# Kernel optimization log

Measured on AMD Instinct MI355X. Metric: run time of the kernel, lower is better.

Reference implementation:

```python
import jax, jax.numpy as jnp
import numpy as np

N = 50000
E = 800000


def _lin(x, w, b):
    return x @ w.T + b


def _gat(h, src, dst, w, a_src, a_dst, b):
    # Single-head PyG-style GATConv (heads=1, negative_slope=0.2), self-loops added by caller.
    n = h.shape[0]
    hw = h @ w.T                                              # [n, out]
    logit = jax.nn.leaky_relu((hw @ a_src)[src] + (hw @ a_dst)[dst], negative_slope=0.2)  # [e]
    m = jax.ops.segment_max(logit, dst, num_segments=n)
    m = jax.lax.stop_gradient(jnp.where(jnp.isfinite(m), m, 0.0))
    ex = jnp.exp(logit - m[dst])
    denom = jax.ops.segment_sum(ex, dst, num_segments=n)
    alpha = ex / (denom[dst] + 1e-16)                          # segment softmax over incoming edges
    return jax.ops.segment_sum(alpha[:, None] * hw[src], dst, num_segments=n) + b


def _forward(x_all, edge_index,
             sep1_w, sep1_b, sep2_w, sep2_b, sep3_w, sep3_b, sep4_w, sep4_b,
             sep5_w, sep5_b, sep6_w, sep6_b, sep7_w, sep7_b, sep8_w, sep8_b,
             conv1_w, conv1_as, conv1_ad, conv1_b,
             conv2_w, conv2_as, conv2_ad, conv2_b,
             conv3_w, conv3_as, conv3_ad, conv3_b,
             lstm_wih, lstm_whh, lstm_bih, lstm_bhh,
             lin1_w, lin1_b, lin2_w, lin2_b, lin3_w, lin3_b):
    n = x_all.shape[0]
    loops = jnp.arange(n)
    src = jnp.concatenate([edge_index[0], loops])  # GATConv default add_self_loops=True
    dst = jnp.concatenate([edge_index[1], loops])
    relu, sig = jax.nn.relu, jax.nn.sigmoid
    xr = relu(_lin(sig(_lin(x_all[:, 1:3],    sep1_w, sep1_b)), sep5_w, sep5_b))   # [n,64]
    xl = relu(_lin(sig(_lin(x_all[:, 3:16],   sep2_w, sep2_b)), sep6_w, sep6_b))   # [n,64]
    xs = relu(_lin(sig(_lin(x_all[:, 16:56],  sep3_w, sep3_b)), sep7_w, sep7_b))   # [n,128]
    xv = relu(_lin(sig(_lin(x_all[:, 56:421], sep4_w, sep4_b)), sep8_w, sep8_b))   # [n,128]
    x = jnp.concatenate([xr, xl, xs, xv], axis=1)                                  # [n,384]
    x = relu(_gat(x, src, dst, conv1_w, conv1_as, conv1_ad, conv1_b))              # [n,128]
    x = relu(_gat(x, src, dst, conv2_w, conv2_as, conv2_ad, conv2_b))              # [n,128]
    x = relu(_gat(x, src, dst, conv3_w, conv3_as, conv3_ad, conv3_b))              # [n,64]
    # LSTM with seq_len=1, h0=c0=0 -> a single cell step; W_hh term vanishes (h0=0)
    t = x_all[:, 421:441]                                                          # [n,20]
    gates = t @ lstm_wih.T + lstm_bih + lstm_bhh                                   # [n,256]
    i, f, g, o = jnp.split(gates, 4, axis=1)                                       # torch gate order i,f,g,o
    c = sig(i) * jnp.tanh(g)
    h = sig(o) * jnp.tanh(c)                                                       # [n,64]
    x = jnp.concatenate([x, h], axis=1)                                            # [n,128]
    x = relu(_lin(x, lin1_w, lin1_b))
    x = relu(_lin(x, lin2_w, lin2_b))
    return _lin(x, lin3_w, lin3_b)                                                 # [n,56]


def setup_inputs() -> dict:
    key = jax.random.key(0)
    ks = iter(jax.random.split(key, 64))
    def w(shape, scale=0.05):
        return jax.random.normal(next(ks), shape, dtype=jnp.float32) * scale
    inp = {
        'x_all': jax.random.normal(next(ks), (N, 441), dtype=jnp.float32),
        'edge_index': jax.random.randint(next(ks), (2, E), 0, N),
        'sep1_w': w((64, 2)),    'sep1_b': w((64,)),
        'sep2_w': w((64, 13)),   'sep2_b': w((64,)),
        'sep3_w': w((128, 40)),  'sep3_b': w((128,)),
        'sep4_w': w((128, 365)), 'sep4_b': w((128,)),
        'sep5_w': w((64, 64)),   'sep5_b': w((64,)),
        'sep6_w': w((64, 64)),   'sep6_b': w((64,)),
        'sep7_w': w((128, 128)), 'sep7_b': w((128,)),
        'sep8_w': w((128, 128)), 'sep8_b': w((128,)),
        'conv1_w': w((128, 384)), 'conv1_as': w((128,)), 'conv1_ad': w((128,)), 'conv1_b': w((128,)),
        'conv2_w': w((128, 128)), 'conv2_as': w((128,)), 'conv2_ad': w((128,)), 'conv2_b': w((128,)),
        'conv3_w': w((64, 128)),  'conv3_as': w((64,)),  'conv3_ad': w((64,)),  'conv3_b': w((64,)),
        'lstm_wih': w((256, 20)), 'lstm_whh': w((256, 64)), 'lstm_bih': w((256,)), 'lstm_bhh': w((256,)),
        'lin1_w': w((64, 128)), 'lin1_b': w((64,)),
        'lin2_w': w((64, 64)),  'lin2_b': w((64,)),
        'lin3_w': w((56, 64)),  'lin3_b': w((56,)),
    }
    return inp


def reference(x_all, edge_index,
              sep1_w, sep1_b, sep2_w, sep2_b, sep3_w, sep3_b, sep4_w, sep4_b,
              sep5_w, sep5_b, sep6_w, sep6_b, sep7_w, sep7_b, sep8_w, sep8_b,
              conv1_w, conv1_as, conv1_ad, conv1_b,
              conv2_w, conv2_as, conv2_ad, conv2_b,
              conv3_w, conv3_as, conv3_ad, conv3_b,
              lstm_wih, lstm_whh, lstm_bih, lstm_bhh,
              lin1_w, lin1_b, lin2_w, lin2_b, lin3_w, lin3_b):
    return _forward(x_all, edge_index,
                    sep1_w, sep1_b, sep2_w, sep2_b, sep3_w, sep3_b, sep4_w, sep4_b,
                    sep5_w, sep5_b, sep6_w, sep6_b, sep7_w, sep7_b, sep8_w, sep8_b,
                    conv1_w, conv1_as, conv1_ad, conv1_b,
                    conv2_w, conv2_as, conv2_ad, conv2_b,
                    conv3_w, conv3_as, conv3_ad, conv3_b,
                    lstm_wih, lstm_whh, lstm_bih, lstm_bhh,
                    lin1_w, lin1_b, lin2_w, lin2_b, lin3_w, lin3_b)
```

## Files before the change

kernel.cpp:

```cpp
#include <hip/hip_runtime.h>
#include <hip/hip_bf16.h>
#include <math.h>

#define N_NODES 50000
#define N_EDGES 800000
#define NP 50048
#define RB16 (NP / 16)

typedef __hip_bfloat16 bf16;
typedef __attribute__((ext_vector_type(8))) short short8;
typedef __attribute__((ext_vector_type(4))) float f32x4;

__device__ __forceinline__ float lrelu(float x) { return x > 0.f ? x : 0.2f * x; }

__device__ __forceinline__ short f2b(float v) {
    bf16 h = __float2bfloat16(v);
    return *reinterpret_cast<short*>(&h);
}
__device__ __forceinline__ float lo_bf(unsigned u) { return __uint_as_float(u << 16); }
__device__ __forceinline__ float hi_bf(unsigned u) { return __uint_as_float(u & 0xFFFF0000u); }
__device__ __forceinline__ float b2f_s(unsigned short s) {
    return __uint_as_float(((unsigned)s) << 16);
}
__device__ __forceinline__ unsigned pack_bf(float v0, float v1) {
    unsigned a = (unsigned)(unsigned short)f2b(v0);
    unsigned b = (unsigned)(unsigned short)f2b(v1);
    return a | (b << 16);
}
__device__ __forceinline__ float sigm(float x) { return 1.f / (1.f + expf(-x)); }

__device__ __forceinline__ size_t fm_idx(int row, int c, int KIo) {
    return ((size_t)(row >> 4) * KIo + (c >> 5)) * 512 +
           (size_t)((c >> 3) & 3) * 128 + (size_t)(row & 15) * 8 + (c & 7);
}

template <int KI, int K, int OFF>
__device__ __forceinline__ void pack_x_body(const float* __restrict__ x,
                                            short* __restrict__ out, int nrows,
                                            long long t)
{
    int lane = (int)(t & 63);
    long long rem = t >> 6;
    int ki = (int)(rem % KI);
    int rb = (int)(rem / KI);
    if (rb >= RB16) return;
    int r = rb * 16 + (lane & 15);
    int kb = ki * 32 + (lane >> 4) * 8;
    short8 tmp;
    if (r < nrows && kb + 8 <= K) {
        const float* p = x + (size_t)r * 441 + OFF + kb;
        f32x4 a = *(const f32x4*)p;
        f32x4 b = *(const f32x4*)(p + 4);
#pragma unroll
        for (int j = 0; j < 4; j++) tmp[j] = f2b(a[j]);
#pragma unroll
        for (int j = 0; j < 4; j++) tmp[4 + j] = f2b(b[j]);
    } else if (r < nrows && kb < K) {
        const float* p = x + (size_t)r * 441 + OFF + kb;
#pragma unroll
        for (int j = 0; j < 8; j++) tmp[j] = (kb + j < K) ? f2b(p[j]) : (short)0;
    } else {
#pragma unroll
        for (int j = 0; j < 8; j++) tmp[j] = 0;
    }
    *(short8*)(out + (((size_t)rb * KI + ki) * 64 + lane) * 8) = tmp;
}

__global__ __launch_bounds__(256) void pack_x2_kernel(
    const float* __restrict__ x, short* __restrict__ xs4,
    short* __restrict__ xs3, int nrows)
{
    long long t = (long long)blockIdx.x * 256 + threadIdx.x;
    const long long T4 = (long long)RB16 * 12 * 64;
    if (t < T4) pack_x_body<12, 365, 56>(x, xs4, nrows, t);
    else        pack_x_body<2, 40, 16>(x, xs3, nrows, t - T4);
}

struct PackDesc {
    const float* src;
    short* dst;
    int lda, M, K, CT, KI;
};
struct PackArgs {
    PackDesc d[16];
    unsigned long long sz[16];
    int n;
};

__global__ __launch_bounds__(256) void pack_all_kernel(PackArgs pa,
                                                       unsigned long long total)
{
    for (unsigned long long i =
             (unsigned long long)blockIdx.x * blockDim.x + threadIdx.x;
         i < total; i += (unsigned long long)gridDim.x * blockDim.x) {
        unsigned long long off = i;
        int s = 0;
        while (s < pa.n - 1 && off >= pa.sz[s]) { off -= pa.sz[s]; s++; }
        PackDesc D = pa.d[s];
        int j = (int)(off & 7);
        int lane = (int)((off >> 3) & 63);
        unsigned rem = (unsigned)(off >> 9);
        int ct = rem % (unsigned)D.CT;
        int ki = rem / (unsigned)D.CT;
        int r = ct * 16 + (lane & 15);
        int k = ki * 32 + (lane >> 4) * 8 + j;
        float v = (r < D.M && k < D.K) ? D.src[(size_t)r * D.lda + k] : 0.f;
        D.dst[off] = f2b(v);
    }
}

template <int ACT, int ODT, int CT, int KI, int SCORES>
__global__ __launch_bounds__(256) void dgemm_kernel(
    const short* __restrict__ A,
    const short* __restrict__ W,
    const float* __restrict__ bias,
    void* __restrict__ Cv, int ldc, int nrows, int M,
    const float* __restrict__ a_src, const float* __restrict__ a_dst,
    float* __restrict__ ssrc, float* __restrict__ sdst)
{
    int tid = threadIdx.x;
    int row0 = blockIdx.x * 64;
    int wv = tid >> 6, lane = tid & 63;
    int lrow = lane & 15, quad = lane >> 4;

    const short* Ap = A + ((size_t)((row0 >> 4) + wv) * KI) * 512 + (size_t)lane * 8;
    const short* Wp = W + (size_t)lane * 8;

    short8 areg[KI];
#pragma unroll
    for (int ki = 0; ki < KI; ki++) areg[ki] = *(const short8*)(Ap + (size_t)ki * 512);

    f32x4 acc[CT];
#pragma unroll
    for (int ct = 0; ct < CT; ct++)
#pragma unroll
        for (int i = 0; i < 4; i++) acc[ct][i] = 0.f;

#pragma unroll
    for (int ki = 0; ki < KI; ki++) {
        short8 breg[CT];
#pragma unroll
        for (int ct = 0; ct < CT; ct++)
            breg[ct] = *(const short8*)(Wp + ((size_t)ki * CT + ct) * 512);
#pragma unroll
        for (int ct = 0; ct < CT; ct++)
            acc[ct] = __builtin_amdgcn_mfma_f32_16x16x32_bf16(areg[ki], breg[ct], acc[ct], 0, 0, 0);
    }

    float* Cf = (float*)Cv;
    bf16*  Cb = (bf16*)Cv;
#pragma unroll
    for (int ct = 0; ct < CT; ct++) {
        int gcol = ct * 16 + lrow;
        if (gcol >= M) continue;
        float bv = bias ? bias[gcol] : 0.f;
#pragma unroll
        for (int i = 0; i < 4; i++) {
            int grow = row0 + wv * 16 + quad * 4 + i;
            if (grow >= nrows) continue;
            float v = acc[ct][i] + bv;
            if (ACT == 1) v = fmaxf(v, 0.f);
            if (ACT == 2) v = sigm(v);
            if (ODT == 1) Cb[(size_t)grow * ldc + gcol] = __float2bfloat16(v);
            else          Cf[(size_t)grow * ldc + gcol] = v;
        }
    }

    if (SCORES) {
        float as_c[CT], ad_c[CT];
#pragma unroll
        for (int ct = 0; ct < CT; ct++) {
            int gcol = ct * 16 + lrow;
            as_c[ct] = (gcol < M) ? a_src[gcol] : 0.f;
            ad_c[ct] = (gcol < M) ? a_dst[gcol] : 0.f;
        }
#pragma unroll
        for (int i = 0; i < 4; i++) {
            float ps = 0.f, pd = 0.f;
#pragma unroll
            for (int ct = 0; ct < CT; ct++) {
                ps = fmaf(acc[ct][i], as_c[ct], ps);
                pd = fmaf(acc[ct][i], ad_c[ct], pd);
            }
#pragma unroll
            for (int off = 8; off > 0; off >>= 1) {
                ps += __shfl_down(ps, off);
                pd += __shfl_down(pd, off);
            }
            if (lrow == 0) {
                int grow = row0 + wv * 16 + quad * 4 + i;
                if (grow < nrows) { ssrc[grow] = ps; sdst[grow] = pd; }
            }
        }
    }
}

template <int ADT, int CT1, int CT2, int KI1>
__device__ __forceinline__ void brmlp_body(
    short* sH,
    const void* __restrict__ Av, int lda, int aoff,
    const short* __restrict__ W1p, const float* __restrict__ B1,
    const short* __restrict__ W2p, const float* __restrict__ B2,
    short* __restrict__ out, int KIo, int coff, int nrows, int K1)
{
    constexpr int M1 = CT1 * 16;
    constexpr int LDH = M1 + 8;
    constexpr int KI2 = M1 / 32;

    int tid = threadIdx.x;
    int row0 = blockIdx.x * 64;
    int wv = tid >> 6, lane = tid & 63;
    int lrow = lane & 15, quad = lane >> 4;

    {
        short8 areg[KI1];
        if (ADT == 1) {
            const short* As = (const short*)Av +
                              ((size_t)((row0 >> 4) + wv) * KI1) * 512 + (size_t)lane * 8;
#pragma unroll
            for (int ki = 0; ki < KI1; ki++)
                areg[ki] = *(const short8*)(As + (size_t)ki * 512);
        } else {
            const float* Af = (const float*)Av;
            int arow = row0 + wv * 16 + lrow;
            bool rok = arow < nrows;
#pragma unroll
            for (int ki = 0; ki < KI1; ki++)
#pragma unroll
                for (int j = 0; j < 8; j++) {
                    int k = ki * 32 + quad * 8 + j;
                    areg[ki][j] = (rok && k < K1)
                                      ? f2b(Af[(size_t)arow * lda + aoff + k])
                                      : (short)0;
                }
        }

        f32x4 acc[CT1];
#pragma unroll
        for (int ct = 0; ct < CT1; ct++)
#pragma unroll
            for (int i = 0; i < 4; i++) acc[ct][i] = 0.f;

#pragma unroll
        for (int ki = 0; ki < KI1; ki++) {
            short8 breg[CT1];
#pragma unroll
            for (int ct = 0; ct < CT1; ct++)
                breg[ct] = *(const short8*)(W1p + ((size_t)ki * CT1 + ct) * 512 +
                                            (size_t)lane * 8);
#pragma unroll
            for (int ct = 0; ct < CT1; ct++)
                acc[ct] = __builtin_amdgcn_mfma_f32_16x16x32_bf16(areg[ki], breg[ct], acc[ct], 0, 0, 0);
        }
#pragma unroll
        for (int ct = 0; ct < CT1; ct++) {
            int col = ct * 16 + lrow;
            float bv = B1[col];
#pragma unroll
            for (int i = 0; i < 4; i++)
                sH[(wv * 16 + quad * 4 + i) * LDH + col] = f2b(sigm(acc[ct][i] + bv));
        }
    }

    {
        f32x4 acc[CT2];
#pragma unroll
        for (int ct = 0; ct < CT2; ct++)
#pragma unroll
            for (int i = 0; i < 4; i++) acc[ct][i] = 0.f;

#pragma unroll
        for (int ki = 0; ki < KI2; ki++) {
            short8 a = *(short8*)&sH[(wv * 16 + lrow) * LDH + ki * 32 + quad * 8];
            short8 breg[CT2];
#pragma unroll
            for (int ct = 0; ct < CT2; ct++)
                breg[ct] = *(const short8*)(W2p + ((size_t)ki * CT2 + ct) * 512 +
                                            (size_t)lane * 8);
#pragma unroll
            for (int ct = 0; ct < CT2; ct++)
                acc[ct] = __builtin_amdgcn_mfma_f32_16x16x32_bf16(a, breg[ct], acc[ct], 0, 0, 0);
        }
#pragma unroll
        for (int ct = 0; ct < CT2; ct++) {
            int gcol = ct * 16 + lrow;
            float bv = B2[gcol];
            int c = coff + gcol;
#pragma unroll
            for (int i = 0; i < 4; i++) {
                int grow = row0 + wv * 16 + quad * 4 + i;
                if (grow >= nrows) continue;
                float v = fmaxf(acc[ct][i] + bv, 0.f);
                out[fm_idx(grow, c, KIo)] = f2b(v);
            }
        }
    }
}

template <int ADT, int CT1, int CT2, int KI1>
__global__ __launch_bounds__(256) void brmlp_kernel(
    const void* __restrict__ Av, int lda, int aoff,
    const short* __restrict__ W1p, const float* __restrict__ B1,
    const short* __restrict__ W2p, const float* __restrict__ B2,
    short* __restrict__ out, int KIo, int coff, int nrows, int K1)
{
    __shared__ short sH[64 * (CT1 * 16 + 8)];
    brmlp_body<ADT, CT1, CT2, KI1>(sH, Av, lda, aoff, W1p, B1, W2p, B2,
                                   out, KIo, coff, nrows, K1);
}

__global__ __launch_bounds__(256) void brmlp_pair_kernel(
    const void* __restrict__ Av, int lda,
    const short* __restrict__ W1a, const float* __restrict__ B1a,
    const short* __restrict__ W2a, const float* __restrict__ B2a,
    const short* __restrict__ W1b, const float* __restrict__ B1b,
    const short* __restrict__ W2b, const float* __restrict__ B2b,
    short* __restrict__ out, int KIo, int nrows)
{
    __shared__ short sH[64 * 72];
    if (blockIdx.y == 0)
        brmlp_body<0, 4, 4, 1>(sH, Av, lda, 1, W1a, B1a, W2a, B2a,
                               out, KIo, 0, nrows, 2);
    else
        brmlp_body<0, 4, 4, 1>(sH, Av, lda, 3, W1b, B1b, W2b, B2b,
                               out, KIo, 64, nrows, 13);
}

__global__ __launch_bounds__(256) void head_kernel(
    const short* __restrict__ xgs, const float* __restrict__ x_all,
    const float* __restrict__ wih, const float* __restrict__ bih,
    const float* __restrict__ bhh,
    const short* __restrict__ w1p, const float* __restrict__ b1,
    const short* __restrict__ w2p, const float* __restrict__ b2,
    const short* __restrict__ w3p, const float* __restrict__ b3,
    float* __restrict__ dout, int n)
{
    __shared__ short sW[20][200];
    __shared__ float sT[64][20];
    __shared__ short sH[64][72];
    __shared__ short sH2[64][72];
    __shared__ short sH3[64][72];

    int tid = threadIdx.x;
    int row0 = blockIdx.x * 64;
    int wv = tid >> 6, lane = tid & 63;
    int lrow = lane & 15, quad = lane >> 4;

    short8 axg[2];
#pragma unroll
    for (int ki = 0; ki < 2; ki++)
        axg[ki] = *(const short8*)(xgs + (((size_t)((row0 >> 4) + wv) * 2 + ki) * 64 +
                                          lane) * 8);

    for (int i = tid; i < 20 * 192; i += 256) {
        int k = i / 192, j = i % 192;
        int gate = j >> 6, jj = j & 63;
        int srow = (gate == 0) ? jj : (gate == 1 ? 128 + jj : 192 + jj);
        sW[k][j] = f2b(wih[srow * 20 + k]);
    }
    for (int i = tid; i < 64 * 20; i += 256) {
        int r = i / 20, k = i % 20;
        int grow = row0 + r;
        sT[r][k] = (grow < n) ? x_all[(size_t)grow * 441 + 421 + k] : 0.f;
    }
    __syncthreads();

    for (int p = 0; p < 16; p++) {
        int idx = p * 256 + tid;
        int r = idx >> 6, j = idx & 63;
        float gi = 0.f, gg = 0.f, go = 0.f;
#pragma unroll
        for (int k = 0; k < 20; k++) {
            float t = sT[r][k];
            gi = fmaf(t, b2f_s((unsigned short)sW[k][j]), gi);
            gg = fmaf(t, b2f_s((unsigned short)sW[k][64 + j]), gg);
            go = fmaf(t, b2f_s((unsigned short)sW[k][128 + j]), go);
        }
        gi += bih[j] + bhh[j];
        gg += bih[128 + j] + bhh[128 + j];
        go += bih[192 + j] + bhh[192 + j];
        float c = sigm(gi) * tanhf(gg);
        float h = sigm(go) * tanhf(c);
        sH[r][j] = f2b(h);
    }
    __syncthreads();

    f32x4 acc[4];
#pragma unroll
    for (int ct = 0; ct < 4; ct++)
#pragma unroll
        for (int i = 0; i < 4; i++) acc[ct][i] = 0.f;
#pragma unroll
    for (int ki = 0; ki < 4; ki++) {
        short8 a = (ki < 2) ? axg[ki]
                            : *(short8*)&sH[wv * 16 + lrow][(ki - 2) * 32 + quad * 8];
        short8 breg[4];
#pragma unroll
        for (int ct = 0; ct < 4; ct++)
            breg[ct] = *(const short8*)(w1p + ((size_t)ki * 4 + ct) * 512 +
                                        (size_t)lane * 8);
#pragma unroll
        for (int ct = 0; ct < 4; ct++)
            acc[ct] = __builtin_amdgcn_mfma_f32_16x16x32_bf16(a, breg[ct], acc[ct], 0, 0, 0);
    }
#pragma unroll
    for (int ct = 0; ct < 4; ct++) {
        int col = ct * 16 + lrow;
        float bv = b1[col];
#pragma unroll
        for (int i = 0; i < 4; i++)
            sH2[wv * 16 + quad * 4 + i][col] = f2b(fmaxf(acc[ct][i] + bv, 0.f));
    }

#pragma unroll
    for (int ct = 0; ct < 4; ct++)
#pragma unroll
        for (int i = 0; i < 4; i++) acc[ct][i] = 0.f;
#pragma unroll
    for (int ki = 0; ki < 2; ki++) {
        short8 a = *(short8*)&sH2[wv * 16 + lrow][ki * 32 + quad * 8];
        short8 breg[4];
#pragma unroll
        for (int ct = 0; ct < 4; ct++)
            breg[ct] = *(const short8*)(w2p + ((size_t)ki * 4 + ct) * 512 +
                                        (size_t)lane * 8);
#pragma unroll
        for (int ct = 0; ct < 4; ct++)
            acc[ct] = __builtin_amdgcn_mfma_f32_16x16x32_bf16(a, breg[ct], acc[ct], 0, 0, 0);
    }
#pragma unroll
    for (int ct = 0; ct < 4; ct++) {
        int col = ct * 16 + lrow;
        float bv = b2[col];
#pragma unroll
        for (int i = 0; i < 4; i++)
            sH3[wv * 16 + quad * 4 + i][col] = f2b(fmaxf(acc[ct][i] + bv, 0.f));
    }

#pragma unroll
    for (int ct = 0; ct < 4; ct++)
#pragma unroll
        for (int i = 0; i < 4; i++) acc[ct][i] = 0.f;
#pragma unroll
    for (int ki = 0; ki < 2; ki++) {
        short8 a = *(short8*)&sH3[wv * 16 + lrow][ki * 32 + quad * 8];
        short8 breg[4];
#pragma unroll
        for (int ct = 0; ct < 4; ct++)
            breg[ct] = *(const short8*)(w3p + ((size_t)ki * 4 + ct) * 512 +
                                        (size_t)lane * 8);
#pragma unroll
        for (int ct = 0; ct < 4; ct++)
            acc[ct] = __builtin_amdgcn_mfma_f32_16x16x32_bf16(a, breg[ct], acc[ct], 0, 0, 0);
    }
#pragma unroll
    for (int ct = 0; ct < 4; ct++) {
        int gcol = ct * 16 + lrow;
        if (gcol >= 56) continue;
        float bv = b3[gcol];
#pragma unroll
        for (int i = 0; i < 4; i++) {
            int grow = row0 + wv * 16 + quad * 4 + i;
            if (grow >= n) continue;
            dout[(size_t)grow * 56 + gcol] = acc[ct][i] + bv;
        }
    }
}

template <int FPL, int KIo>
__global__ __launch_bounds__(256) void gat_fused_kernel(
    const bf16* __restrict__ hw, const int* __restrict__ rowptr,
    const int* __restrict__ colidx, const float* __restrict__ ss,
    const float* __restrict__ sd, const float* __restrict__ bias,
    short* __restrict__ out, int n, int F)
{
    int wv = threadIdx.x >> 6, lane = threadIdx.x & 63;
    int node = blockIdx.x * 4 + wv;
    if (node >= n) return;
    const unsigned short* hwu = (const unsigned short*)hw;
    float sdn = sd[node];
    float wself = expf(lrelu(ss[node] + sdn));
    float a0, a1 = 0.f;
    if (FPL == 2) {
        unsigned u = *(const unsigned*)(hwu + (size_t)node * F + 2 * lane);
        a0 = wself * lo_bf(u);
        a1 = wself * hi_bf(u);
    } else {
        a0 = wself * b2f_s(hwu[(size_t)node * F + lane]);
    }
    int e0 = rowptr[node];
    int deg = rowptr[node + 1] - e0;
    float den_l = 0.f;
    for (int c0 = 0; c0 < deg; c0 += 64) {
        int mye = c0 + lane;
        int s = 0;
        float w = 0.f;
        if (mye < deg) {
            s = colidx[e0 + mye];
            w = expf(lrelu(ss[s] + sdn));
        }
        den_l += w;
        int cnt = min(64, deg - c0);
        int j = 0;
        for (; j + 7 < cnt; j += 8) {
            int sx[8];
            float wx[8];
#pragma unroll
            for (int q = 0; q < 8; q++) {
                sx[q] = __shfl(s, j + q);
                wx[q] = __shfl(w, j + q);
            }
            if (FPL == 2) {
                unsigned ux[8];
#pragma unroll
                for (int q = 0; q < 8; q++)
                    ux[q] = *(const unsigned*)(hwu + (size_t)sx[q] * F + 2 * lane);
#pragma unroll
                for (int q = 0; q < 8; q++) {
                    a0 = fmaf(wx[q], lo_bf(ux[q]), a0);
                    a1 = fmaf(wx[q], hi_bf(ux[q]), a1);
                }
            } else {
                float hx[8];
#pragma unroll
                for (int q = 0; q < 8; q++)
                    hx[q] = b2f_s(hwu[(size_t)sx[q] * F + lane]);
#pragma unroll
                for (int q = 0; q < 8; q++) a0 = fmaf(wx[q], hx[q], a0);
            }
        }
        for (; j + 3 < cnt; j += 4) {
            int s0 = __shfl(s, j), s1 = __shfl(s, j + 1);
            int s2 = __shfl(s, j + 2), s3 = __shfl(s, j + 3);
            float w0 = __shfl(w, j), w1v = __shfl(w, j + 1);
            float w2v = __shfl(w, j + 2), w3v = __shfl(w, j + 3);
            if (FPL == 2) {
                unsigned u0 = *(const unsigned*)(hwu + (size_t)s0 * F + 2 * lane);
                unsigned u1 = *(const unsigned*)(hwu + (size_t)s1 * F + 2 * lane);
                unsigned u2 = *(const unsigned*)(hwu + (size_t)s2 * F + 2 * lane);
                unsigned u3 = *(const unsigned*)(hwu + (size_t)s3 * F + 2 * lane);
                a0 = fmaf(w0, lo_bf(u0), a0);  a1 = fmaf(w0, hi_bf(u0), a1);
                a0 = fmaf(w1v, lo_bf(u1), a0); a1 = fmaf(w1v, hi_bf(u1), a1);
                a0 = fmaf(w2v, lo_bf(u2), a0); a1 = fmaf(w2v, hi_bf(u2), a1);
                a0 = fmaf(w3v, lo_bf(u3), a0); a1 = fmaf(w3v, hi_bf(u3), a1);
            } else {
                float h0 = b2f_s(hwu[(size_t)s0 * F + lane]);
                float h1 = b2f_s(hwu[(size_t)s1 * F + lane]);
                float h2 = b2f_s(hwu[(size_t)s2 * F + lane]);
                float h3 = b2f_s(hwu[(size_t)s3 * F + lane]);
                a0 = fmaf(w0, h0, a0);
                a0 = fmaf(w1v, h1, a0);
                a0 = fmaf(w2v, h2, a0);
                a0 = fmaf(w3v, h3, a0);
            }
        }
        for (; j < cnt; j++) {
            int s0 = __shfl(s, j);
            float w0 = __shfl(w, j);
            if (FPL == 2) {
                unsigned u0 = *(const unsigned*)(hwu + (size_t)s0 * F + 2 * lane);
                a0 = fmaf(w0, lo_bf(u0), a0);
                a1 = fmaf(w0, hi_bf(u0), a1);
            } else {
                a0 = fmaf(w0, b2f_s(hwu[(size_t)s0 * F + lane]), a0);
            }
        }
    }
#pragma unroll
    for (int off = 32; off > 0; off >>= 1) den_l += __shfl_xor(den_l, off);
    float inv = 1.f / (den_l + wself);
    int rb = node >> 4, nr = node & 15;
    if (FPL == 2) {
        float v0 = fmaxf(a0 * inv + bias[2 * lane], 0.f);
        float v1 = fmaxf(a1 * inv + bias[2 * lane + 1], 0.f);
        size_t uidx = ((size_t)rb * KIo + (lane >> 4)) * 256 +
                      (size_t)((lane >> 2) & 3) * 64 + nr * 4 + (lane & 3);
        ((unsigned*)out)[uidx] = pack_bf(v0, v1);
    } else {
        float v0 = fmaxf(a0 * inv + bias[lane], 0.f);
        size_t sidx = ((size_t)rb * KIo + (lane >> 5)) * 512 +
                      (size_t)((lane >> 3) & 3) * 128 + nr * 8 + (lane & 7);
        out[sidx] = f2b(v0);
    }
}

__global__ void count_kernel(const int* __restrict__ dst, int* __restrict__ cnt,
                             int e)
{
    for (int i = blockIdx.x * blockDim.x + threadIdx.x; i < e;
         i += gridDim.x * blockDim.x)
        atomicAdd(cnt + dst[i], 1);
}

#define SCAN_BLOCKS 256

__global__ __launch_bounds__(256) void scan_local_kernel(
    const int* __restrict__ cnt, int* __restrict__ rowptr,
    int* __restrict__ bsum, int n, int chunk)
{
    __shared__ int tmp[256];
    int b = blockIdx.x, tid = threadIdx.x;
    int i = b * chunk + tid;
    int v = (tid < chunk && i < n) ? cnt[i] : 0;
    tmp[tid] = v;
    __syncthreads();
    for (int off = 1; off < 256; off <<= 1) {
        int t = (tid >= off) ? tmp[tid - off] : 0;
        __syncthreads();
        tmp[tid] += t;
        __syncthreads();
    }
    if (tid < chunk && i < n) rowptr[i] = tmp[tid] - v;
    if (tid == 255) bsum[b] = tmp[255];
}

__global__ __launch_bounds__(256) void scan_bsums_kernel(
    int* __restrict__ bsum, int* __restrict__ rowptr, int n)
{
    __shared__ int tmp[256];
    int tid = threadIdx.x;
    int v = bsum[tid];
    tmp[tid] = v;
    __syncthreads();
    for (int off = 1; off < 256; off <<= 1) {
        int t = (tid >= off) ? tmp[tid - off] : 0;
        __syncthreads();
        tmp[tid] += t;
        __syncthreads();
    }
    bsum[tid] = tmp[tid] - v;
    if (tid == 255) rowptr[n] = tmp[255];
}

__global__ __launch_bounds__(256) void scan_add_kernel(
    int* __restrict__ rowptr, int* __restrict__ nextp,
    const int* __restrict__ bsum, int n, int chunk)
{
    int b = blockIdx.x, tid = threadIdx.x;
    int i = b * chunk + tid;
    if (tid < chunk && i < n) {
        int v = rowptr[i] + bsum[b];
        rowptr[i] = v;
        nextp[i] = v;
    }
}

__global__ void fill_kernel(const int* __restrict__ src,
                            const int* __restrict__ dst,
                            int* __restrict__ nextp, int* __restrict__ colidx,
                            int e)
{
    for (int i = blockIdx.x * blockDim.x + threadIdx.x; i < e;
         i += gridDim.x * blockDim.x) {
        int pos = atomicAdd(nextp + dst[i], 1);
        colidx[pos] = src[i];
    }
}

extern "C" void kernel_launch(void* const* d_in, const int* in_sizes, int n_in,
                              void* d_out, int out_size, void* d_ws,
                              size_t ws_size, hipStream_t stream)
{
    const int N = N_NODES;
    const int E = N_EDGES;

    const float* x_all = (const float*)d_in[0];
    const int* edges = (const int*)d_in[1];
    const int* e_src = edges;
    const int* e_dst = edges + E;

    const float* sep1_w = (const float*)d_in[2];  const float* sep1_b = (const float*)d_in[3];
    const float* sep2_w = (const float*)d_in[4];  const float* sep2_b = (const float*)d_in[5];
    const float* sep3_w = (const float*)d_in[6];  const float* sep3_b = (const float*)d_in[7];
    const float* sep4_w = (const float*)d_in[8];  const float* sep4_b = (const float*)d_in[9];
    const float* sep5_w = (const float*)d_in[10]; const float* sep5_b = (const float*)d_in[11];
    const float* sep6_w = (const float*)d_in[12]; const float* sep6_b = (const float*)d_in[13];
    const float* sep7_w = (const float*)d_in[14]; const float* sep7_b = (const float*)d_in[15];
    const float* sep8_w = (const float*)d_in[16]; const float* sep8_b = (const float*)d_in[17];
    const float* conv1_w = (const float*)d_in[18];
    const float* conv1_as = (const float*)d_in[19];
    const float* conv1_ad = (const float*)d_in[20];
    const float* conv1_b = (const float*)d_in[21];
    const float* conv2_w = (const float*)d_in[22];
    const float* conv2_as = (const float*)d_in[23];
    const float* conv2_ad = (const float*)d_in[24];
    const float* conv2_b = (const float*)d_in[25];
    const float* conv3_w = (const float*)d_in[26];
    const float* conv3_as = (const float*)d_in[27];
    const float* conv3_ad = (const float*)d_in[28];
    const float* conv3_b = (const float*)d_in[29];
    const float* lstm_wih = (const float*)d_in[30];
    const float* lstm_bih = (const float*)d_in[32];
    const float* lstm_bhh = (const float*)d_in[33];
    const float* lin1_w = (const float*)d_in[34]; const float* lin1_b = (const float*)d_in[35];
    const float* lin2_w = (const float*)d_in[36]; const float* lin2_b = (const float*)d_in[37];
    const float* lin3_w = (const float*)d_in[38]; const float* lin3_b = (const float*)d_in[39];

    char* ws = (char*)d_ws;
    size_t off = 0;
    auto alloc = [&](size_t bytes) {
        void* p = ws + off;
        off += (bytes + 255) & ~(size_t)255;
        return p;
    };
    short* x0 = (short*)alloc((size_t)NP * 384 * 2);
    short* Bb = (short*)alloc((size_t)NP * 128 * 2);
    float* ssrc = (float*)alloc((size_t)N * 4);
    float* sdst = (float*)alloc((size_t)N * 4);
    int* rowptr = (int*)alloc((size_t)(N + 1) * 4);
    int* nextp  = (int*)alloc((size_t)N * 4);
    int* cnt    = (int*)alloc((size_t)N * 4);
    int* bsum   = (int*)alloc((size_t)SCAN_BLOCKS * 4);
    int* colidx = (int*)alloc((size_t)E * 4);

    short* conv1p = (short*)alloc((size_t)128 * 384 * 2);
    short* conv2p = (short*)alloc((size_t)128 * 128 * 2);
    short* conv3p = (short*)alloc((size_t)64 * 128 * 2);
    short* sep1p  = (short*)alloc((size_t)64 * 32 * 2);
    short* sep2p  = (short*)alloc((size_t)64 * 32 * 2);
    short* sep3p  = (short*)alloc((size_t)128 * 64 * 2);
    short* sep4p  = (short*)alloc((size_t)128 * 384 * 2);
    short* sep5p  = (short*)alloc((size_t)64 * 64 * 2);
    short* sep6p  = (short*)alloc((size_t)64 * 64 * 2);
    short* sep7p  = (short*)alloc((size_t)128 * 128 * 2);
    short* sep8p  = (short*)alloc((size_t)128 * 128 * 2);
    short* lin1p  = (short*)alloc((size_t)64 * 128 * 2);
    short* lin2p  = (short*)alloc((size_t)64 * 64 * 2);
    short* lin3p  = (short*)alloc((size_t)64 * 64 * 2);

    size_t need_xs = off + (size_t)NP * 64 * 2 + (size_t)NP * 384 * 2 + 1024;
    bool packx = ws_size >= need_xs;
    short* xs3 = packx ? (short*)alloc((size_t)NP * 64 * 2) : nullptr;
    short* xs4 = packx ? (short*)alloc((size_t)NP * 384 * 2) : nullptr;

    short* C  = x0;
    short* xg = x0;

    dim3 blk(256);
    int gx = NP / 64;
    int nb4 = (N + 3) / 4;
    int chunk = (N + SCAN_BLOCKS - 1) / SCAN_BLOCKS;

    hipMemsetAsync(cnt, 0, (size_t)N * 4, stream);
    count_kernel<<<1024, 256, 0, stream>>>(e_dst, cnt, E);
    scan_local_kernel<<<SCAN_BLOCKS, 256, 0, stream>>>(cnt, rowptr, bsum, N, chunk);
    scan_bsums_kernel<<<1, 256, 0, stream>>>(bsum, rowptr, N);
    scan_add_kernel<<<SCAN_BLOCKS, 256, 0, stream>>>(rowptr, nextp, bsum, N, chunk);
    fill_kernel<<<1024, 256, 0, stream>>>(e_src, e_dst, nextp, colidx, E);

    if (packx) {
        long long tot = (long long)RB16 * 14 * 64;
        pack_x2_kernel<<<(int)((tot + 255) / 256), blk, 0, stream>>>(
            x_all, xs4, xs3, N);
    }
    {
        PackArgs pa{};
        unsigned long long total = 0;
        int np = 0;
        auto addp = [&](const float* src, short* dst, int lda, int M, int K,
                        int CT, int KI) {
            pa.d[np].src = src; pa.d[np].dst = dst; pa.d[np].lda = lda;
            pa.d[np].M = M; pa.d[np].K = K; pa.d[np].CT = CT; pa.d[np].KI = KI;
            pa.sz[np] = (unsigned long long)CT * KI * 512;
            total += pa.sz[np];
            np++;
        };
        addp(conv1_w, conv1p, 384, 128, 384, 8, 12);
        addp(sep4_w, sep4p, 365, 128, 365, 8, 12);
        addp(conv2_w, conv2p, 128, 128, 128, 8, 4);
        addp(sep7_w, sep7p, 128, 128, 128, 8, 4);
        addp(sep8_w, sep8p, 128, 128, 128, 8, 4);
        addp(conv3_w, conv3p, 128, 64, 128, 4, 4);
        addp(lin1_w, lin1p, 128, 64, 128, 4, 4);
        addp(sep3_w, sep3p, 40, 128, 40, 8, 2);
        addp(sep5_w, sep5p, 64, 64, 64, 4, 2);
        addp(sep6_w, sep6p, 64, 64, 64, 4, 2);
        addp(lin2_w, lin2p, 64, 64, 64, 4, 2);
        addp(lin3_w, lin3p, 64, 56, 64, 4, 2);
        addp(sep1_w, sep1p, 2, 64, 2, 4, 1);
        addp(sep2_w, sep2p, 13, 64, 13, 4, 1);
        pa.n = np;
        pack_all_kernel<<<512, 256, 0, stream>>>(pa, total);
    }

    brmlp_pair_kernel<<<dim3(gx, 2), blk, 0, stream>>>(
        x_all, 441, sep1p, sep1_b, sep5p, sep5_b,
        sep2p, sep2_b, sep6p, sep6_b, x0, 12, N);
    if (packx) {
        brmlp_kernel<1, 8, 8, 2><<<gx, blk, 0, stream>>>(
            xs3, 64, 0, sep3p, sep3_b, sep7p, sep7_b, x0, 12, 128, N, 64);
        brmlp_kernel<1, 8, 8, 12><<<gx, blk, 0, stream>>>(
            xs4, 384, 0, sep4p, sep4_b, sep8p, sep8_b, x0, 12, 256, N, 384);
    } else {
        brmlp_kernel<0, 8, 8, 2><<<gx, blk, 0, stream>>>(
            x_all, 441, 16, sep3p, sep3_b, sep7p, sep7_b, x0, 12, 128, N, 40);
        brmlp_kernel<0, 8, 8, 12><<<gx, blk, 0, stream>>>(
            x_all, 441, 56, sep4p, sep4_b, sep8p, sep8_b, x0, 12, 256, N, 365);
    }

    dgemm_kernel<0, 1, 8, 12, 1><<<gx, blk, 0, stream>>>(
        x0, conv1p, nullptr, Bb, 128, N, 128,
        conv1_as, conv1_ad, ssrc, sdst);
    gat_fused_kernel<2, 4><<<nb4, 256, 0, stream>>>(
        (const bf16*)Bb, rowptr, colidx, ssrc, sdst, conv1_b, C, N, 128);

    dgemm_kernel<0, 1, 8, 4, 1><<<gx, blk, 0, stream>>>(
        C, conv2p, nullptr, Bb, 128, N, 128,
        conv2_as, conv2_ad, ssrc, sdst);
    gat_fused_kernel<2, 4><<<nb4, 256, 0, stream>>>(
        (const bf16*)Bb, rowptr, colidx, ssrc, sdst, conv2_b, C, N, 128);

    dgemm_kernel<0, 1, 4, 4, 1><<<gx, blk, 0, stream>>>(
        C, conv3p, nullptr, Bb, 64, N, 64,
        conv3_as, conv3_ad, ssrc, sdst);
    gat_fused_kernel<1, 2><<<nb4, 256, 0, stream>>>(
        (const bf16*)Bb, rowptr, colidx, ssrc, sdst, conv3_b, xg, N, 64);

    head_kernel<<<gx, blk, 0, stream>>>(
        xg, x_all, lstm_wih, lstm_bih, lstm_bhh,
        lin1p, lin1_b, lin2p, lin2_b, lin3p, lin3_b,
        (float*)d_out, N);
}
```

Measured before the change: 564.6 us.

## Build CSR via two-level bucket partition instead of global atomic counting sort

Replaces the global-atomic count, three-pass scan and scatter-fill CSR build with a bucketed approach. A shared-memory histogram over 256-node buckets and a single-block scan are followed by a partition of (src,dst) pairs into buckets. A per-bucket kernel then does a local count, scan and scatter into colidx. This targets the cost of global atomics and scattered writes. It needs an extra 8-byte-per-edge pairs buffer and only runs when workspace allows, otherwise it falls back to the old path.

```diff
diff --git a/kernel.cpp b/kernel.cpp
--- a/kernel.cpp
+++ b/kernel.cpp
@@ -6,6 +6,7 @@
 #define N_EDGES 800000
 #define NP 50048
 #define RB16 (NP / 16)
+#define NB 196
 
 typedef __hip_bfloat16 bf16;
 typedef __attribute__((ext_vector_type(8))) short short8;
@@ -581,6 +582,111 @@
         size_t sidx = ((size_t)rb * KIo + (lane >> 5)) * 512 +
                       (size_t)((lane >> 3) & 3) * 128 + nr * 8 + (lane & 7);
         out[sidx] = f2b(v0);
+    }
+}
+
+__global__ __launch_bounds__(256) void bhist_kernel(const int* __restrict__ dst,
+                                                    int* __restrict__ bcnt, int e)
+{
+    __shared__ int l[NB];
+    for (int i = threadIdx.x; i < NB; i += 256) l[i] = 0;
+    __syncthreads();
+    for (int i = blockIdx.x * blockDim.x + threadIdx.x; i < e;
+         i += gridDim.x * blockDim.x)
+        atomicAdd(&l[dst[i] >> 8], 1);
+    __syncthreads();
+    for (int i = threadIdx.x; i < NB; i += 256)
+        if (l[i]) atomicAdd(&bcnt[i], l[i]);
+}
+
+__global__ __launch_bounds__(256) void bscan_kernel(
+    const int* __restrict__ bcnt, int* __restrict__ boff,
+    int* __restrict__ bcur, int* __restrict__ rowptr, int n, int e)
+{
+    __shared__ int tmp[256];
+    int tid = threadIdx.x;
+    int v = (tid < NB) ? bcnt[tid] : 0;
+    tmp[tid] = v;
+    __syncthreads();
+    for (int off = 1; off < 256; off <<= 1) {
+        int t = (tid >= off) ? tmp[tid - off] : 0;
+        __syncthreads();
+        tmp[tid] += t;
+        __syncthreads();
+    }
+    int excl = tmp[tid] - v;
+    if (tid < NB) { boff[tid] = excl; bcur[tid] = excl; }
+    if (tid == 0) { boff[NB] = e; rowptr[n] = e; }
+}
+
+__global__ __launch_bounds__(256) void bpart_kernel(
+    const int* __restrict__ src, const int* __restrict__ dst,
+    int* __restrict__ bcur, int2* __restrict__ pairs, int e)
+{
+    __shared__ int lcnt[NB];
+    __shared__ int lbase[NB];
+    const int TILE = 2048;
+    for (long long t0 = (long long)blockIdx.x * TILE; t0 < e;
+         t0 += (long long)gridDim.x * TILE) {
+        for (int i = threadIdx.x; i < NB; i += 256) lcnt[i] = 0;
+        __syncthreads();
+        int rank[8], bb[8], sv[8], dv[8];
+#pragma unroll
+        for (int k = 0; k < 8; k++) {
+            int i = (int)t0 + k * 256 + threadIdx.x;
+            bb[k] = -1;
+            if (i < e) {
+                int d = dst[i];
+                sv[k] = src[i];
+                dv[k] = d;
+                bb[k] = d >> 8;
+                rank[k] = atomicAdd(&lcnt[bb[k]], 1);
+            }
+        }
+        __syncthreads();
+        for (int i = threadIdx.x; i < NB; i += 256)
+            lbase[i] = lcnt[i] ? atomicAdd(&bcur[i], lcnt[i]) : 0;
+        __syncthreads();
+#pragma unroll
+        for (int k = 0; k < 8; k++)
+            if (bb[k] >= 0)
+                pairs[(size_t)lbase[bb[k]] + rank[k]] = make_int2(sv[k], dv[k]);
+        __syncthreads();
+    }
+}
+
+__global__ __launch_bounds__(256) void bcsr_kernel(
+    const int2* __restrict__ pairs, const int* __restrict__ boff,
+    int* __restrict__ rowptr, int* __restrict__ colidx, int n)
+{
+    __shared__ int ncnt[256];
+    __shared__ int tmp[256];
+    int tid = threadIdx.x, b = blockIdx.x;
+    int base = boff[b], end = boff[b + 1];
+    ncnt[tid] = 0;
+    __syncthreads();
+    for (int i = base + tid; i < end; i += 256)
+        atomicAdd(&ncnt[pairs[i].y & 255], 1);
+    __syncthreads();
+    int v = ncnt[tid];
+    tmp[tid] = v;
+    __syncthreads();
+    for (int off = 1; off < 256; off <<= 1) {
+        int t = (tid >= off) ? tmp[tid - off] : 0;
+        __syncthreads();
+        tmp[tid] += t;
+        __syncthreads();
+    }
+    int excl = base + tmp[tid] - v;
+    int node = (b << 8) + tid;
+    if (node < n) rowptr[node] = excl;
+    __syncthreads();
+    ncnt[tid] = excl;
+    __syncthreads();
+    for (int i = base + tid; i < end; i += 256) {
+        int2 p = pairs[i];
+        int pos = atomicAdd(&ncnt[p.y & 255], 1);
+        colidx[pos] = p.x;
     }
 }
 
@@ -712,6 +818,9 @@
     int* cnt    = (int*)alloc((size_t)N * 4);
     int* bsum   = (int*)alloc((size_t)SCAN_BLOCKS * 4);
     int* colidx = (int*)alloc((size_t)E * 4);
+    int* bcnt   = (int*)alloc((size_t)NB * 4);
+    int* boff   = (int*)alloc((size_t)(NB + 1) * 4);
+    int* bcur   = (int*)alloc((size_t)NB * 4);
 
     short* conv1p = (short*)alloc((size_t)128 * 384 * 2);
     short* conv2p = (short*)alloc((size_t)128 * 128 * 2);
@@ -733,20 +842,33 @@
     short* xs3 = packx ? (short*)alloc((size_t)NP * 64 * 2) : nullptr;
     short* xs4 = packx ? (short*)alloc((size_t)NP * 384 * 2) : nullptr;
 
+    size_t need_pairs = off + (size_t)E * 8 + 1024;
+    bool binfill = ws_size >= need_pairs;
+    int2* pairs = binfill ? (int2*)alloc((size_t)E * 8) : nullptr;
+
     short* C  = x0;
     short* xg = x0;
 
     dim3 blk(256);
     int gx = NP / 64;
     int nb4 = (N + 3) / 4;
-    int chunk = (N + SCAN_BLOCKS - 1) / SCAN_BLOCKS;
-
-    hipMemsetAsync(cnt, 0, (size_t)N * 4, stream);
-    count_kernel<<<1024, 256, 0, stream>>>(e_dst, cnt, E);
-    scan_local_kernel<<<SCAN_BLOCKS, 256, 0, stream>>>(cnt, rowptr, bsum, N, chunk);
-    scan_bsums_kernel<<<1, 256, 0, stream>>>(bsum, rowptr, N);
-    scan_add_kernel<<<SCAN_BLOCKS, 256, 0, stream>>>(rowptr, nextp, bsum, N, chunk);
-    fill_kernel<<<1024, 256, 0, stream>>>(e_src, e_dst, nextp, colidx, E);
+
+    if (binfill) {
+        hipMemsetAsync(bcnt, 0, (size_t)NB * 4, stream);
+        bhist_kernel<<<1024, 256, 0, stream>>>(e_dst, bcnt, E);
+        bscan_kernel<<<1, 256, 0, stream>>>(bcnt, boff, bcur, rowptr, N, E);
+        bpart_kernel<<<(E + 2047) / 2048, 256, 0, stream>>>(e_src, e_dst, bcur,
+                                                            pairs, E);
+        bcsr_kernel<<<NB, 256, 0, stream>>>(pairs, boff, rowptr, colidx, N);
+    } else {
+        int chunk = (N + SCAN_BLOCKS - 1) / SCAN_BLOCKS;
+        hipMemsetAsync(cnt, 0, (size_t)N * 4, stream);
+        count_kernel<<<1024, 256, 0, stream>>>(e_dst, cnt, E);
+        scan_local_kernel<<<SCAN_BLOCKS, 256, 0, stream>>>(cnt, rowptr, bsum, N, chunk);
+        scan_bsums_kernel<<<1, 256, 0, stream>>>(bsum, rowptr, N);
+        scan_add_kernel<<<SCAN_BLOCKS, 256, 0, stream>>>(rowptr, nextp, bsum, N, chunk);
+        fill_kernel<<<1024, 256, 0, stream>>>(e_src, e_dst, nextp, colidx, E);
+    }
 
     if (packx) {
         long long tot = (long long)RB16 * 14 * 64;
```

Result: faster. 511.0 us (-9.5%).
